# Kernel optimization log

Measured on AMD Instinct MI355X. Metric: run time of the kernel, lower is better.

Reference implementation:

```python
import jax, jax.numpy as jnp
import numpy as np

K = 7        # local attention window (kernel_size)
PAD = 3      # (K-1)//2, keeps spatial dims
GROUPS = 8   # attention heads


def _unfold(t, k, H, W):
    """t: [B,C,H+k-1,W+k-1] -> [B,C,H,W,k,k] sliding-window patches (stride 1).
    Matches torch .unfold(2,k,1).unfold(3,k,1): first k over height offsets,
    second k over width offsets."""
    cols = [t[:, :, i:i + H, j:j + W] for i in range(k) for j in range(k)]
    p = jnp.stack(cols, axis=-1)  # [B,C,H,W,k*k]
    return p.reshape(t.shape[0], t.shape[1], H, W, k, k)


def setup_inputs() -> dict:
    key = jax.random.key(0)
    ks = jax.random.split(key, 6)
    B, C, O, H, Wd = 4, 128, 128, 64, 64
    x = jax.random.normal(ks[0], (B, C, H, Wd), dtype=jnp.float32)
    # 1x1 conv weights, kaiming normal fan_out (fan_out = O for 1x1)
    scale = (2.0 / O) ** 0.5
    Wq = jax.random.normal(ks[1], (O, C), dtype=jnp.float32) * scale
    Wk = jax.random.normal(ks[2], (O, C), dtype=jnp.float32) * scale
    Wv = jax.random.normal(ks[3], (O, C), dtype=jnp.float32) * scale
    rel_h = jax.random.normal(ks[4], (O // 2, 1, 1, K, 1), dtype=jnp.float32)
    rel_w = jax.random.normal(ks[5], (O // 2, 1, 1, 1, K), dtype=jnp.float32)
    return {"x": x, "Wq": Wq, "Wk": Wk, "Wv": Wv, "rel_h": rel_h, "rel_w": rel_w}


def reference(x, Wq, Wk, Wv, rel_h, rel_w):
    B, C, H, W = x.shape
    O = Wq.shape[0]
    g = GROUPS
    # 1x1 convs (no bias)
    q = jnp.einsum('bchw,oc->bohw', x, Wq)                    # [B,O,H,W]
    xp = jnp.pad(x, ((0, 0), (0, 0), (PAD, PAD), (PAD, PAD)))
    k = jnp.einsum('bchw,oc->bohw', xp, Wk)                   # [B,O,Hp,Wp]
    v = jnp.einsum('bchw,oc->bohw', xp, Wv)
    kp = _unfold(k, K, H, W)                                  # [B,O,H,W,K,K]
    vp = _unfold(v, K, H, W)
    # relative position embeddings: height on first half of channels, width on second
    kh, kw = jnp.split(kp, 2, axis=1)
    kp = jnp.concatenate([kh + rel_h, kw + rel_w], axis=1)    # [B,O,H,W,K,K]
    kp = kp.reshape(B, g, O // g, H, W, K * K)
    vp = vp.reshape(B, g, O // g, H, W, K * K)
    qg = q.reshape(B, g, O // g, H, W, 1)
    scores = (qg * kp).sum(axis=2)                            # [B,g,H,W,K*K]
    attn = jax.nn.softmax(scores, axis=-1)
    out = jnp.einsum('bghwn,bgchwn->bgchw', attn, vp)         # [B,g,O/g,H,W]
    return out.reshape(B, O, H, W)
```

## Files before the change

### kernel.cpp

```cpp
#include <hip/hip_runtime.h>
#include <hip/hip_bf16.h>

#define B_   4
#define C_   128
#define H_   64
#define W_   64
#define HW_  4096
#define KW_  7
#define PAD_ 3
#define G_   8
#define CPG_ 16

#define CPAD 136

#define TS    16
#define HALO  22
#define NHP   (HALO*HALO)
#define LP    24

typedef _Float16 f16x8 __attribute__((ext_vector_type(8)));
typedef float    f32x4 __attribute__((ext_vector_type(4)));

static __device__ __forceinline__ unsigned short f2h(float f) {
    _Float16 h = (_Float16)f;
    union { _Float16 h; unsigned short u; } cv; cv.h = h;
    return cv.u;
}

__global__ __launch_bounds__(256) void proj_mfma(
    const float* __restrict__ x,
    const float* __restrict__ Wq,
    const float* __restrict__ Wk,
    const float* __restrict__ Wv,
    unsigned short* __restrict__ qkv16)
{
    const int ptile = blockIdx.x;
    const int b     = blockIdx.y;
    const int m     = blockIdx.z;
    const float* Wm = (m == 0) ? Wq : ((m == 1) ? Wk : Wv);
    const float* xb = x + (size_t)b * C_ * HW_;
    unsigned short* y = qkv16 + ((size_t)(m * B_ + b)) * HW_ * C_;
    const int p0  = ptile * 128;
    const int tid = threadIdx.x;

    __shared__ unsigned short wls[128 * CPAD];
    __shared__ unsigned short xls[128 * CPAD];

    #pragma unroll
    for (int it = 0; it < 16; ++it) {
        const int idx = tid + it * 256;
        const int o   = idx >> 5;
        const int c4  = (idx & 31) * 4;
        const float4 w4 = *(const float4*)(Wm + (size_t)o * C_ + c4);
        ushort4 hh;
        hh.x = f2h(w4.x); hh.y = f2h(w4.y); hh.z = f2h(w4.z); hh.w = f2h(w4.w);
        *(ushort4*)(&wls[o * CPAD + c4]) = hh;
    }
    #pragma unroll
    for (int it = 0; it < 4; ++it) {
        const int idx = tid + it * 256;
        const int cq  = (idx >> 5) * 4;
        const int pq  = (idx & 31) * 4;
        const float* xp = xb + (size_t)cq * HW_ + p0 + pq;
        const float4 r0 = *(const float4*)(xp);
        const float4 r1 = *(const float4*)(xp + HW_);
        const float4 r2 = *(const float4*)(xp + 2 * HW_);
        const float4 r3 = *(const float4*)(xp + 3 * HW_);
        ushort4 hh;
        hh.x = f2h(r0.x); hh.y = f2h(r1.x); hh.z = f2h(r2.x); hh.w = f2h(r3.x);
        *(ushort4*)(&xls[(pq + 0) * CPAD + cq]) = hh;
        hh.x = f2h(r0.y); hh.y = f2h(r1.y); hh.z = f2h(r2.y); hh.w = f2h(r3.y);
        *(ushort4*)(&xls[(pq + 1) * CPAD + cq]) = hh;
        hh.x = f2h(r0.z); hh.y = f2h(r1.z); hh.z = f2h(r2.z); hh.w = f2h(r3.z);
        *(ushort4*)(&xls[(pq + 2) * CPAD + cq]) = hh;
        hh.x = f2h(r0.w); hh.y = f2h(r1.w); hh.z = f2h(r2.w); hh.w = f2h(r3.w);
        *(ushort4*)(&xls[(pq + 3) * CPAD + cq]) = hh;
    }
    __syncthreads();

    const int wv   = tid >> 6;
    const int lane = tid & 63;
    const int row  = lane & 15;
    const int kq   = lane >> 4;

    f32x4 acc[2][8];
    #pragma unroll
    for (int pt = 0; pt < 2; ++pt)
        #pragma unroll
        for (int ot = 0; ot < 8; ++ot)
            acc[pt][ot] = (f32x4){0.f, 0.f, 0.f, 0.f};

    #pragma unroll
    for (int ks = 0; ks < 4; ++ks) {
        const int cb = ks * 32 + kq * 8;
        const f16x8 b0 = *(const f16x8*)(&xls[(wv * 32 +      row) * CPAD + cb]);
        const f16x8 b1 = *(const f16x8*)(&xls[(wv * 32 + 16 + row) * CPAD + cb]);
        #pragma unroll
        for (int ot = 0; ot < 8; ++ot) {
            const f16x8 af = *(const f16x8*)(&wls[(ot * 16 + row) * CPAD + cb]);
            acc[0][ot] = __builtin_amdgcn_mfma_f32_16x16x32_f16(af, b0, acc[0][ot], 0, 0, 0);
            acc[1][ot] = __builtin_amdgcn_mfma_f32_16x16x32_f16(af, b1, acc[1][ot], 0, 0, 0);
        }
    }

    const int pbase = p0 + wv * 32;
    #pragma unroll
    for (int pt = 0; pt < 2; ++pt) {
        const int p = pbase + pt * 16 + row;
        #pragma unroll
        for (int ot = 0; ot < 8; ++ot) {
            ushort4 hh;
            hh.x = f2h(acc[pt][ot][0]); hh.y = f2h(acc[pt][ot][1]);
            hh.z = f2h(acc[pt][ot][2]); hh.w = f2h(acc[pt][ot][3]);
            *(ushort4*)(y + ((size_t)ot * HW_ + p) * CPG_ + kq * 4) = hh;
        }
    }
}

__global__ __launch_bounds__(256) void attn_kernel(
    const unsigned short* __restrict__ qkv16,
    const float* __restrict__ rel_h,
    const float* __restrict__ rel_w,
    float* __restrict__ out)
{
    const int tile = blockIdx.x;
    const int g    = blockIdx.y;
    const int b    = blockIdx.z;
    const int h0   = (tile >> 2) * TS;
    const int w0   = (tile & 3) * TS;
    const int c0   = g * CPG_;

    __shared__ unsigned short kvls[2][NHP * LP];

    const size_t gplane = (size_t)HW_ * CPG_;
    const size_t mplane = (size_t)B_ * G_ * gplane;
    const unsigned short* qb = qkv16              + ((size_t)b * G_ + g) * gplane;
    const unsigned short* kb = qkv16 + mplane     + ((size_t)b * G_ + g) * gplane;
    const unsigned short* vb = qkv16 + 2 * mplane + ((size_t)b * G_ + g) * gplane;

    const int tid = threadIdx.x;

    #pragma unroll
    for (int it = 0; it < 8; ++it) {
        const int idx = tid + it * 256;
        if (idx < 2 * NHP * 2) {
            const int arr  = (idx >= NHP * 2) ? 1 : 0;
            const int r    = idx - arr * NHP * 2;
            const int lp   = r >> 1;
            const int half = r & 1;
            const int hy   = h0 + lp / HALO - PAD_;
            const int hx   = w0 + lp % HALO - PAD_;
            f16x8 val = (f16x8)(_Float16)0.f;
            if ((unsigned)hy < (unsigned)H_ && (unsigned)hx < (unsigned)W_) {
                const unsigned short* src = (arr ? vb : kb)
                    + (size_t)(hy * W_ + hx) * CPG_ + half * 8;
                val = *(const f16x8*)src;
            }
            *(f16x8*)(&kvls[arr][lp * LP + half * 8]) = val;
        }
    }
    __syncthreads();

    const int pw  = tid & 15;
    const int ph  = tid >> 4;
    const int pix = (h0 + ph) * W_ + (w0 + pw);

    float qv[CPG_];
    {
        const f16x8 q0 = *(const f16x8*)(qb + (size_t)pix * CPG_);
        const f16x8 q1 = *(const f16x8*)(qb + (size_t)pix * CPG_ + 8);
        #pragma unroll
        for (int c = 0; c < 8; ++c) { qv[c] = (float)q0[c]; qv[8 + c] = (float)q1[c]; }
    }

    const bool useH = (g < 4);
    const float* rp = useH ? (rel_h + c0 * KW_) : (rel_w + (c0 - 64) * KW_);
    float rel[KW_];
    #pragma unroll
    for (int t = 0; t < KW_; ++t) {
        float r = 0.f;
        #pragma unroll
        for (int c = 0; c < CPG_; ++c) r += qv[c] * rp[c * KW_ + t];
        rel[t] = r;
    }

    float s[KW_ * KW_];
    float smax = -1e30f;
    #pragma unroll
    for (int i = 0; i < KW_; ++i) {
        #pragma unroll
        for (int j = 0; j < KW_; ++j) {
            const unsigned short* kp = &kvls[0][((ph + i) * HALO + (pw + j)) * LP];
            const f16x8 k0 = *(const f16x8*)(kp);
            const f16x8 k1 = *(const f16x8*)(kp + 8);
            float sc = useH ? rel[i] : rel[j];
            #pragma unroll
            for (int c = 0; c < 8; ++c)
                sc += qv[c] * (float)k0[c] + qv[8 + c] * (float)k1[c];
            s[i * KW_ + j] = sc;
            smax = fmaxf(smax, sc);
        }
    }

    float denom = 0.f;
    #pragma unroll
    for (int n = 0; n < KW_ * KW_; ++n) {
        s[n] = __expf(s[n] - smax);
        denom += s[n];
    }
    const float rdenom = 1.f / denom;

    float acc[CPG_];
    #pragma unroll
    for (int c = 0; c < CPG_; ++c) acc[c] = 0.f;
    #pragma unroll
    for (int i = 0; i < KW_; ++i) {
        #pragma unroll
        for (int j = 0; j < KW_; ++j) {
            const float a = s[i * KW_ + j];
            const unsigned short* vp = &kvls[1][((ph + i) * HALO + (pw + j)) * LP];
            const f16x8 v0 = *(const f16x8*)(vp);
            const f16x8 v1 = *(const f16x8*)(vp + 8);
            #pragma unroll
            for (int c = 0; c < 8; ++c) {
                acc[c]     += a * (float)v0[c];
                acc[8 + c] += a * (float)v1[c];
            }
        }
    }

    float* ob = out + ((size_t)b * C_ + c0) * HW_;
    #pragma unroll
    for (int c = 0; c < CPG_; ++c)
        ob[(size_t)c * HW_ + pix] = acc[c] * rdenom;
}

extern "C" void kernel_launch(void* const* d_in, const int* in_sizes, int n_in,
                              void* d_out, int out_size, void* d_ws, size_t ws_size,
                              hipStream_t stream) {
    const float* x     = (const float*)d_in[0];
    const float* Wq    = (const float*)d_in[1];
    const float* Wk    = (const float*)d_in[2];
    const float* Wv    = (const float*)d_in[3];
    const float* rel_h = (const float*)d_in[4];
    const float* rel_w = (const float*)d_in[5];
    unsigned short* ws = (unsigned short*)d_ws;
    float* out = (float*)d_out;

    dim3 gA(HW_ / 128, B_, 3);
    proj_mfma<<<gA, 256, 0, stream>>>(x, Wq, Wk, Wv, ws);

    dim3 gB(16, G_, B_);
    attn_kernel<<<gB, 256, 0, stream>>>(ws, rel_h, rel_w, out);
}
```

Before: 35.79 us.

## Pre-convert weights to fp16 once and halve projection pixel tile

Adds a small kernel that converts Wq/Wk/Wv to fp16 once into workspace. The projection kernel then reads weight fragments straight from global/L2 instead of staging a converted copy in LDS per block, and processes 64 pixels per block instead of 128. This removes redundant per-block weight conversion and LDS traffic and doubles the block count for better occupancy. In exchange it adds an extra kernel launch, and the MFMA A operands become global loads that depend on cache hits.

```diff
diff --git a/kernel.cpp b/kernel.cpp
--- a/kernel.cpp
+++ b/kernel.cpp
@@ -27,40 +27,43 @@
     return cv.u;
 }
 
-__global__ __launch_bounds__(256) void proj_mfma(
-    const float* __restrict__ x,
+__global__ __launch_bounds__(256) void w16_kernel(
     const float* __restrict__ Wq,
     const float* __restrict__ Wk,
     const float* __restrict__ Wv,
+    unsigned short* __restrict__ w16)
+{
+    const int gid = blockIdx.x * 256 + threadIdx.x;
+    const int m   = gid >> 12;
+    const int r   = gid & 4095;
+    const float* src = (m == 0) ? Wq : ((m == 1) ? Wk : Wv);
+    const float4 v = *(const float4*)(src + (size_t)r * 4);
+    ushort4 hh;
+    hh.x = f2h(v.x); hh.y = f2h(v.y); hh.z = f2h(v.z); hh.w = f2h(v.w);
+    *(ushort4*)(w16 + ((size_t)m << 14) + (size_t)r * 4) = hh;
+}
+
+__global__ __launch_bounds__(256) void proj_mfma(
+    const float* __restrict__ x,
+    const unsigned short* __restrict__ w16,
     unsigned short* __restrict__ qkv16)
 {
     const int ptile = blockIdx.x;
     const int b     = blockIdx.y;
     const int m     = blockIdx.z;
-    const float* Wm = (m == 0) ? Wq : ((m == 1) ? Wk : Wv);
+    const unsigned short* wm = w16 + ((size_t)m << 14);
     const float* xb = x + (size_t)b * C_ * HW_;
     unsigned short* y = qkv16 + ((size_t)(m * B_ + b)) * HW_ * C_;
-    const int p0  = ptile * 128;
+    const int p0  = ptile * 64;
     const int tid = threadIdx.x;
 
-    __shared__ unsigned short wls[128 * CPAD];
-    __shared__ unsigned short xls[128 * CPAD];
-
-    #pragma unroll
-    for (int it = 0; it < 16; ++it) {
+    __shared__ unsigned short xls[64 * CPAD];
+
+    #pragma unroll
+    for (int it = 0; it < 2; ++it) {
         const int idx = tid + it * 256;
-        const int o   = idx >> 5;
-        const int c4  = (idx & 31) * 4;
-        const float4 w4 = *(const float4*)(Wm + (size_t)o * C_ + c4);
-        ushort4 hh;
-        hh.x = f2h(w4.x); hh.y = f2h(w4.y); hh.z = f2h(w4.z); hh.w = f2h(w4.w);
-        *(ushort4*)(&wls[o * CPAD + c4]) = hh;
-    }
-    #pragma unroll
-    for (int it = 0; it < 4; ++it) {
-        const int idx = tid + it * 256;
-        const int cq  = (idx >> 5) * 4;
-        const int pq  = (idx & 31) * 4;
+        const int pq  = (idx & 15) * 4;
+        const int cq  = (idx >> 4) * 4;
         const float* xp = xb + (size_t)cq * HW_ + p0 + pq;
         const float4 r0 = *(const float4*)(xp);
         const float4 r1 = *(const float4*)(xp + HW_);
@@ -83,37 +86,29 @@
     const int row  = lane & 15;
     const int kq   = lane >> 4;
 
-    f32x4 acc[2][8];
-    #pragma unroll
-    for (int pt = 0; pt < 2; ++pt)
-        #pragma unroll
-        for (int ot = 0; ot < 8; ++ot)
-            acc[pt][ot] = (f32x4){0.f, 0.f, 0.f, 0.f};
+    f32x4 acc[8];
+    #pragma unroll
+    for (int ot = 0; ot < 8; ++ot)
+        acc[ot] = (f32x4){0.f, 0.f, 0.f, 0.f};
 
     #pragma unroll
     for (int ks = 0; ks < 4; ++ks) {
         const int cb = ks * 32 + kq * 8;
-        const f16x8 b0 = *(const f16x8*)(&xls[(wv * 32 +      row) * CPAD + cb]);
-        const f16x8 b1 = *(const f16x8*)(&xls[(wv * 32 + 16 + row) * CPAD + cb]);
+        const f16x8 bfrag = *(const f16x8*)(&xls[(wv * 16 + row) * CPAD + cb]);
         #pragma unroll
         for (int ot = 0; ot < 8; ++ot) {
-            const f16x8 af = *(const f16x8*)(&wls[(ot * 16 + row) * CPAD + cb]);
-            acc[0][ot] = __builtin_amdgcn_mfma_f32_16x16x32_f16(af, b0, acc[0][ot], 0, 0, 0);
-            acc[1][ot] = __builtin_amdgcn_mfma_f32_16x16x32_f16(af, b1, acc[1][ot], 0, 0, 0);
-        }
-    }
-
-    const int pbase = p0 + wv * 32;
-    #pragma unroll
-    for (int pt = 0; pt < 2; ++pt) {
-        const int p = pbase + pt * 16 + row;
-        #pragma unroll
-        for (int ot = 0; ot < 8; ++ot) {
-            ushort4 hh;
-            hh.x = f2h(acc[pt][ot][0]); hh.y = f2h(acc[pt][ot][1]);
-            hh.z = f2h(acc[pt][ot][2]); hh.w = f2h(acc[pt][ot][3]);
-            *(ushort4*)(y + ((size_t)ot * HW_ + p) * CPG_ + kq * 4) = hh;
-        }
+            const f16x8 afrag = *(const f16x8*)(wm + (size_t)(ot * 16 + row) * C_ + cb);
+            acc[ot] = __builtin_amdgcn_mfma_f32_16x16x32_f16(afrag, bfrag, acc[ot], 0, 0, 0);
+        }
+    }
+
+    const int p = p0 + wv * 16 + row;
+    #pragma unroll
+    for (int ot = 0; ot < 8; ++ot) {
+        ushort4 hh;
+        hh.x = f2h(acc[ot][0]); hh.y = f2h(acc[ot][1]);
+        hh.z = f2h(acc[ot][2]); hh.w = f2h(acc[ot][3]);
+        *(ushort4*)(y + ((size_t)ot * HW_ + p) * CPG_ + kq * 4) = hh;
     }
 }
 
@@ -244,12 +239,16 @@
     const float* Wv    = (const float*)d_in[3];
     const float* rel_h = (const float*)d_in[4];
     const float* rel_w = (const float*)d_in[5];
-    unsigned short* ws = (unsigned short*)d_ws;
+    unsigned short* ws   = (unsigned short*)d_ws;
+    unsigned short* qkv  = ws;
+    unsigned short* w16  = ws + (size_t)3 * B_ * HW_ * C_;
     float* out = (float*)d_out;
 
-    dim3 gA(HW_ / 128, B_, 3);
-    proj_mfma<<<gA, 256, 0, stream>>>(x, Wq, Wk, Wv, ws);
+    w16_kernel<<<48, 256, 0, stream>>>(Wq, Wk, Wv, w16);
+
+    dim3 gA(HW_ / 64, B_, 3);
+    proj_mfma<<<gA, 256, 0, stream>>>(x, w16, qkv);
 
     dim3 gB(16, G_, B_);
-    attn_kernel<<<gB, 256, 0, stream>>>(ws, rel_h, rel_w, out);
-}
+    attn_kernel<<<gB, 256, 0, stream>>>(qkv, rel_h, rel_w, out);
+}
```

Result: slower. 47.52 us (+32.8%).
